# Kernel tuning notes

Measured on AMD Instinct MI355X. Metric: run time of the kernel, lower is better.

## Reference

```python
import jax, jax.numpy as jnp
import numpy as np

B, T, C = 4, 2048, 2048
N_HEAD, N_KV = 16, 4
HEAD_DIM = C // N_HEAD          # 128
KV_DIM = HEAD_DIM * N_KV        # 512
WINDOW = 256
ROPE_BASE = 10000.0


def setup_inputs() -> dict:
    key = jax.random.key(0)
    ks = jax.random.split(key, 5)
    s = 0.02
    return {
        "x": jax.random.normal(ks[0], (B, T, C), dtype=jnp.float32),
        "Wq": jax.random.normal(ks[1], (C, C), dtype=jnp.float32) * s,
        "Wk": jax.random.normal(ks[2], (C, KV_DIM), dtype=jnp.float32) * s,
        "Wv": jax.random.normal(ks[3], (C, KV_DIM), dtype=jnp.float32) * s,
        "Wo": jax.random.normal(ks[4], (C, C), dtype=jnp.float32) * s,
    }


def _rope(x):
    # x: [B, H, T, D]; GPT-NeoX half-split rotation
    d = x.shape[-1]
    t = x.shape[-2]
    inv_freq = 1.0 / (ROPE_BASE ** (jnp.arange(0, d, 2, dtype=jnp.float32) / d))
    freqs = jnp.arange(t, dtype=jnp.float32)[:, None] * inv_freq[None, :]  # [T, D/2]
    cos, sin = jnp.cos(freqs), jnp.sin(freqs)
    x1, x2 = x[..., : d // 2], x[..., d // 2:]
    return jnp.concatenate([x1 * cos - x2 * sin, x1 * sin + x2 * cos], axis=-1)


def reference(x, Wq, Wk, Wv, Wo):
    b, t, c = x.shape
    hd = HEAD_DIM
    q = (x @ Wq).reshape(b, t, N_HEAD, hd).transpose(0, 2, 1, 3)   # [B,nh,T,hd]
    k = (x @ Wk).reshape(b, t, N_KV, hd).transpose(0, 2, 1, 3)     # [B,nkv,T,hd]
    v = (x @ Wv).reshape(b, t, N_KV, hd).transpose(0, 2, 1, 3)

    q = _rope(q)
    k = _rope(k)

    # GQA: repeat kv heads to match query heads
    rep = N_HEAD // N_KV
    k = jnp.repeat(k, rep, axis=1)   # [B,nh,T,hd]
    v = jnp.repeat(v, rep, axis=1)

    att = jnp.einsum("bhqd,bhkd->bhqk", q, k) / jnp.sqrt(jnp.float32(hd))
    i = jnp.arange(t)[:, None]
    j = jnp.arange(t)[None, :]
    # causal AND sliding window: i - WINDOW <= j <= i
    mask = (j <= i) & (j >= i - WINDOW)
    att = jnp.where(mask[None, None], att, jnp.finfo(att.dtype).min)
    att = jax.nn.softmax(att, axis=-1)

    y = jnp.einsum("bhqk,bhkd->bhqd", att, v)          # [B,nh,T,hd]
    y = y.transpose(0, 2, 1, 3).reshape(b, t, c)       # [B,T,C]
    return y @ Wo
```

## Files before the change

### kernel.cpp

```cpp
#include <hip/hip_runtime.h>
#include <stdint.h>

#define T_ 2048
#define C_ 2048
#define HD 128
#define LDQKV 3072

typedef unsigned short u16;
typedef __attribute__((ext_vector_type(8))) short bf16x8;
typedef __attribute__((ext_vector_type(4))) float f32x4;
typedef __attribute__((ext_vector_type(4))) float float4v;
typedef __attribute__((ext_vector_type(4))) u16 u16x4;
typedef __attribute__((ext_vector_type(8))) u16 u16x8;

typedef __attribute__((address_space(3))) void lds_void;
typedef const __attribute__((address_space(1))) void gbl_void;

__device__ __forceinline__ void gload_lds16(const void* g, void* l) {
  __builtin_amdgcn_global_load_lds((gbl_void*)(uintptr_t)g,
                                   (lds_void*)(uint32_t)(uintptr_t)l, 16, 0, 0);
}

__device__ __forceinline__ u16 f2bf(float f) {
  union { float f; uint32_t u; } v; v.f = f;
  uint32_t r = v.u + 0x7FFFu + ((v.u >> 16) & 1u);
  return (u16)(r >> 16);
}
__device__ __forceinline__ float bf2f(u16 h) {
  union { uint32_t u; float f; } v; v.u = ((uint32_t)h) << 16;
  return v.f;
}

#define BAR() do { asm volatile("" ::: "memory"); __builtin_amdgcn_s_barrier(); asm volatile("" ::: "memory"); } while (0)
#define VMCNT(n) asm volatile("s_waitcnt vmcnt(" #n ")" ::: "memory")
template<int N> __device__ __forceinline__ void VMCNT_C() {
  if constexpr (N == 0) { VMCNT(0); }
  else if constexpr (N == 3) { VMCNT(3); }
  else if constexpr (N == 4) { VMCNT(4); }
  else { static_assert(N == 0 || N == 3 || N == 4, "add literal"); }
}

__global__ __launch_bounds__(256) void k_conv_x(const float* __restrict__ x, u16* __restrict__ o) {
  size_t idx = (size_t)blockIdx.x * 256 + threadIdx.x;
  float4v xv = *(const float4v*)(x + idx * 4);
  u16x4 r;
#pragma unroll
  for (int e = 0; e < 4; ++e) r[e] = f2bf(xv[e]);
  *(u16x4*)(o + idx * 4) = r;
}

__device__ __forceinline__ void ttile(const float* __restrict__ src, int ldw, int nb,
                                      int k0, int n0out, u16* __restrict__ out, int tid,
                                      float (*Lt)[68]) {
  int kr = tid >> 4, nc = (tid & 15) * 4;
#pragma unroll
  for (int s = 0; s < 4; ++s) {
    float4v v = *(const float4v*)(src + (size_t)(k0 + kr + 16 * s) * ldw + nb + nc);
#pragma unroll
    for (int e = 0; e < 4; ++e) Lt[kr + 16 * s][nc + e] = v[e];
  }
  __syncthreads();
  int nr = tid & 31, kc = (tid >> 5) * 8;
#pragma unroll
  for (int s2 = 0; s2 < 2; ++s2) {
    int n = nr + 32 * s2;
    u16x8 o;
#pragma unroll
    for (int e = 0; e < 8; ++e) o[e] = f2bf(Lt[kc + e][n]);
    *(u16x8*)(out + (size_t)(n0out + n) * 2048 + k0 + kc) = o;
  }
}

__global__ __launch_bounds__(256) void k_wt_qkv(const float* __restrict__ Wq, const float* __restrict__ Wk,
                                                const float* __restrict__ Wv, u16* __restrict__ wt) {
  __shared__ float Lt[64][68];
  const int n0 = blockIdx.x * 64, k0 = blockIdx.y * 64;
  const float* src; int ldw, nb;
  if (n0 < 2048)      { src = Wq; ldw = 2048; nb = n0; }
  else if (n0 < 2560) { src = Wk; ldw = 512;  nb = n0 - 2048; }
  else                { src = Wv; ldw = 512;  nb = n0 - 2560; }
  ttile(src, ldw, nb, k0, n0, wt, threadIdx.x, Lt);
}

__global__ __launch_bounds__(256) void k_wo_t(const float* __restrict__ Wo, u16* __restrict__ wt) {
  __shared__ float Lt[64][68];
  ttile(Wo, 2048, blockIdx.x * 64, blockIdx.y * 64, blockIdx.x * 64, wt, threadIdx.x, Lt);
}

__global__ __launch_bounds__(256) void k_cs(float* __restrict__ cst) {
  int idx = blockIdx.x * 256 + threadIdx.x;
  int t = idx >> 6, d = idx & 63;
  float inv = expf(-(float)d * (1.0f / 64.0f) * 9.2103403719761836f);
  float f = (float)t * inv;
  float s, c;
  sincosf(f, &s, &c);
  cst[idx * 2] = c;
  cst[idx * 2 + 1] = s;
}

__global__ __launch_bounds__(256) void k_rope(u16* __restrict__ qkv, const float* __restrict__ cst) {
  int idx = blockIdx.x * 256 + threadIdx.x;
  int token = idx / 160;
  int rem = idx - token * 160;
  int hd = rem >> 3, oct = rem & 7;
  int col = ((hd < 16) ? hd * 128 : 2048 + (hd - 16) * 128) + oct * 8;
  size_t base = (size_t)token * LDQKV + col;
  int t = token & (T_ - 1);
  float sc = (hd < 16) ? 0.08838834764831845f : 1.0f;
  u16x8 a = *(const u16x8*)(qkv + base);
  u16x8 b2 = *(const u16x8*)(qkv + base + 64);
  const float* cp = cst + (size_t)(t * 64 + oct * 8) * 2;
  u16x8 ra, rb;
#pragma unroll
  for (int e = 0; e < 8; ++e) {
    float c = cp[e * 2], s = cp[e * 2 + 1];
    float x1 = bf2f(a[e]), x2 = bf2f(b2[e]);
    ra[e] = f2bf((x1 * c - x2 * s) * sc);
    rb[e] = f2bf((x1 * s + x2 * c) * sc);
  }
  *(u16x8*)(qkv + base) = ra;
  *(u16x8*)(qkv + base + 64) = rb;
}

template<int OUTF32, int NF>
__global__ __launch_bounds__(512, 1) void k_gemm8(const u16* __restrict__ A, const u16* __restrict__ Bt,
                                                  void* __restrict__ Cout, int M, int N, int K, int nbx) {
  constexpr int BUFE = 16384 + NF * 4096;
  __shared__ __attribute__((aligned(16))) u16 lds[2 * BUFE];
  const int tid = threadIdx.x, lane = tid & 63;
  const int w = tid >> 6, wm = w >> 2, wn = w & 3;
  const int l15 = lane & 15, lhi = lane >> 4;
  const int nwg = gridDim.x, cpx = nwg >> 3;
  const int wg = (blockIdx.x & 7) * cpx + (blockIdx.x >> 3);
  const int bx = wg % nbx, by = wg / nbx;
  const int m0 = by * 256, n0 = bx * (NF * 64);
  const int NT = K >> 6;

  const int srow = tid >> 3;
  const int scol = ((tid & 7) ^ (srow & 7)) * 8;
  const u16* pA0 = A + (size_t)(m0 + srow) * K + scol;
  const u16* pA1 = pA0 + (size_t)64 * K;
  const u16* pA2 = pA0 + (size_t)128 * K;
  const u16* pA3 = pA0 + (size_t)192 * K;
  const u16* pB0 = Bt + (size_t)(n0 + srow) * K + scol;
  const u16* pB1 = pB0 + (size_t)64 * K;
  const u16* pB2 = pB0 + (size_t)128 * K;
  const u16* pB3 = pB0 + (size_t)(NF == 4 ? 192 : 128) * K;
  u16* dEA = lds + tid * 8;
  u16* dEB = lds + 16384 + tid * 8;
  u16* dOA = lds + BUFE + tid * 8;
  u16* dOB = lds + BUFE + 16384 + tid * 8;
  const int xk0 = (lhi ^ (l15 & 7)) * 8;
  const int xk1 = ((4 + lhi) ^ (l15 & 7)) * 8;
  const u16* rAe0 = lds + (wm * 128 + l15) * 64 + xk0;
  const u16* rAe1 = lds + (wm * 128 + l15) * 64 + xk1;
  const u16* rBe0 = lds + 16384 + (wn * (NF * 16) + l15) * 64 + xk0;
  const u16* rBe1 = lds + 16384 + (wn * (NF * 16) + l15) * 64 + xk1;
  const u16* rAo0 = rAe0 + BUFE;
  const u16* rAo1 = rAe1 + BUFE;
  const u16* rBo0 = rBe0 + BUFE;
  const u16* rBo1 = rBe1 + BUFE;

  f32x4 acc[8][NF];
#pragma unroll
  for (int i = 0; i < 8; ++i)
#pragma unroll
    for (int j = 0; j < NF; ++j) acc[i][j] = (f32x4){0.f, 0.f, 0.f, 0.f};

  gload_lds16(pA0, dEA);         gload_lds16(pA1, dEA + 4096);
  gload_lds16(pA2, dEA + 8192);  gload_lds16(pA3, dEA + 12288);
  gload_lds16(pB0, dEB);         gload_lds16(pB1, dEB + 4096);
  gload_lds16(pB2, dEB + 8192);
  if constexpr (NF == 4) gload_lds16(pB3, dEB + 12288);
  pB0 += 64; pB1 += 64; pB2 += 64;
  if constexpr (NF == 4) pB3 += 64;
  gload_lds16(pB0, dOB);         gload_lds16(pB1, dOB + 4096);
  gload_lds16(pB2, dOB + 8192);
  if constexpr (NF == 4) gload_lds16(pB3, dOB + 12288);
  VMCNT_C<NF>();
  BAR();

  auto TILE = [&](const u16* rA0, const u16* rA1, const u16* rB0, const u16* rB1,
                  u16* dA, u16* dB, bool stA, bool nlast) {
    bf16x8 bb[NF][2], aa[4][2];
    auto MH = [&](int h) {
#pragma unroll
      for (int ks = 0; ks < 2; ++ks)
#pragma unroll
        for (int mi = 0; mi < 4; ++mi)
#pragma unroll
          for (int nf = 0; nf < NF; ++nf)
            acc[h * 4 + mi][nf] = __builtin_amdgcn_mfma_f32_16x16x32_bf16(
                aa[mi][ks], bb[nf][ks], acc[h * 4 + mi][nf], 0, 0, 0);
    };
#pragma unroll
    for (int nf = 0; nf < NF; ++nf) {
      bb[nf][0] = *(const bf16x8*)(rB0 + nf * 1024);
      bb[nf][1] = *(const bf16x8*)(rB1 + nf * 1024);
    }
#pragma unroll
    for (int mi = 0; mi < 4; ++mi) {
      aa[mi][0] = *(const bf16x8*)(rA0 + mi * 1024);
      aa[mi][1] = *(const bf16x8*)(rA1 + mi * 1024);
    }
    if (stA) {
      pA0 += 64; pA1 += 64; pA2 += 64; pA3 += 64;
      gload_lds16(pA0, dA);        gload_lds16(pA1, dA + 4096);
      gload_lds16(pA2, dA + 8192); gload_lds16(pA3, dA + 12288);
    }
    __builtin_amdgcn_s_setprio(1);
    MH(0);
    __builtin_amdgcn_s_setprio(0);
    BAR();
#pragma unroll
    for (int mi = 0; mi < 4; ++mi) {
      aa[mi][0] = *(const bf16x8*)(rA0 + 4096 + mi * 1024);
      aa[mi][1] = *(const bf16x8*)(rA1 + 4096 + mi * 1024);
    }
    if (nlast) {
      pB0 += 64; pB1 += 64; pB2 += 64;
      gload_lds16(pB0, dB);        gload_lds16(pB1, dB + 4096);
      gload_lds16(pB2, dB + 8192);
      if constexpr (NF == 4) { pB3 += 64; gload_lds16(pB3, dB + 12288); }
    }
    __builtin_amdgcn_s_setprio(1);
    MH(1);
    __builtin_amdgcn_s_setprio(0);
    if (nlast) { VMCNT_C<NF>(); } else { VMCNT_C<0>(); }
    BAR();
  };

  for (int t = 0; t < NT; t += 2) {
    const bool nlast = (t + 2 < NT);
    TILE(rAe0, rAe1, rBe0, rBe1, dOA, dEB, true,  nlast);
    TILE(rAo0, rAo1, rBo0, rBo1, dEA, dOB, nlast, nlast);
  }

#pragma unroll
  for (int mf = 0; mf < 8; ++mf) {
#pragma unroll
    for (int nf = 0; nf < NF; ++nf) {
      int col = n0 + wn * (NF * 16) + nf * 16 + l15;
#pragma unroll
      for (int r = 0; r < 4; ++r) {
        int row = m0 + wm * 128 + mf * 16 + lhi * 4 + r;
        float v = acc[mf][nf][r];
        if (OUTF32) ((float*)Cout)[(size_t)row * N + col] = v;
        else        ((u16*)Cout)[(size_t)row * N + col] = f2bf(v);
      }
    }
  }
}

__global__ __launch_bounds__(256) void k_attn(const u16* __restrict__ qkv, u16* __restrict__ y) {
  const int bid = blockIdx.x;
  const int qt = bid & 31, h = (bid >> 5) & 15, b = bid >> 9;
  const int i0 = qt * 64;
  const size_t tb = (size_t)b * T_ * LDQKV;
  const u16* qb = qkv + tb + h * HD;
  const u16* kb = qkv + tb + 2048 + (h >> 2) * HD;
  const u16* vb = kb + 512;
  __shared__ __attribute__((aligned(16))) u16 smem[20480];
  u16* Ks = smem;
  u16* Vt = smem + 8192;
  u16* Psw = smem + 16384;
  u16* Qs = smem;
  const int tid = threadIdx.x, lane = tid & 63, w = tid >> 6;
  const int l15 = lane & 15, lhi = lane >> 4;
  u16* Ps = Psw + w * 1024;

#pragma unroll
  for (int it = 0; it < 4; ++it) {
    int c = it * 256 + tid, row = c >> 4, kc = (c & 15) ^ (row & 7);
    gload_lds16(qb + (size_t)(i0 + row) * LDQKV + kc * 8, &Qs[(it * 256 + w * 64) * 8]);
  }
  __syncthreads();
  bf16x8 qf[4];
#pragma unroll
  for (int ks = 0; ks < 4; ++ks) {
    int row = w * 16 + l15;
    int kc = (ks * 4 + lhi) ^ (row & 7);
    qf[ks] = *(const bf16x8*)&Qs[(row * 16 + kc) * 8];
  }
  __syncthreads();

  f32x4 o[8];
#pragma unroll
  for (int dt = 0; dt < 8; ++dt) o[dt] = (f32x4){0.f, 0.f, 0.f, 0.f};
  float mrun[4], lrun[4];
#pragma unroll
  for (int r = 0; r < 4; ++r) { mrun[r] = -1e30f; lrun[r] = 0.f; }

  const int jb0 = (i0 >= 256) ? (i0 - 256) : 0;
  for (int jb = jb0; jb <= i0; jb += 64) {
#pragma unroll
    for (int it = 0; it < 4; ++it) {
      int c = it * 256 + tid, row = c >> 4, kc = (c & 15) ^ (row & 7);
      gload_lds16(kb + (size_t)(jb + row) * LDQKV + kc * 8, &Ks[(it * 256 + w * 64) * 8]);
    }
#pragma unroll
    for (int it = 0; it < 4; ++it) {
      int chunk = it * 256 + tid, row = chunk >> 4, dc = chunk & 15;
      u16x8 vv = *(const u16x8*)(vb + (size_t)(jb + row) * LDQKV + dc * 8);
#pragma unroll
      for (int e = 0; e < 8; ++e) {
        int d = dc * 8 + e;
        int s = (dc ^ e) & 7;
        Vt[d * 64 + (row ^ (s << 3))] = vv[e];
      }
    }
    __syncthreads();

    f32x4 s[4];
#pragma unroll
    for (int t = 0; t < 4; ++t) {
      s[t] = (f32x4){0.f, 0.f, 0.f, 0.f};
#pragma unroll
      for (int ks = 0; ks < 4; ++ks) {
        int row = t * 16 + l15;
        int kc = (ks * 4 + lhi) ^ (row & 7);
        bf16x8 kf = *(const bf16x8*)&Ks[(row * 16 + kc) * 8];
        s[t] = __builtin_amdgcn_mfma_f32_16x16x32_bf16(qf[ks], kf, s[t], 0, 0, 0);
      }
    }

    const int irow0 = i0 + w * 16 + lhi * 4;
    float rmax[4];
#pragma unroll
    for (int r = 0; r < 4; ++r) rmax[r] = -1e30f;
#pragma unroll
    for (int t = 0; t < 4; ++t) {
      int j = jb + t * 16 + l15;
#pragma unroll
      for (int r = 0; r < 4; ++r) {
        int i = irow0 + r;
        float sv = s[t][r];
        sv = (j <= i && j + 256 >= i) ? sv : -1e30f;
        s[t][r] = sv;
        rmax[r] = fmaxf(rmax[r], sv);
      }
    }
#pragma unroll
    for (int r = 0; r < 4; ++r) {
#pragma unroll
      for (int off = 1; off < 16; off <<= 1)
        rmax[r] = fmaxf(rmax[r], __shfl_xor(rmax[r], off));
    }
    float sf[4], psum[4];
#pragma unroll
    for (int r = 0; r < 4; ++r) {
      float mn = fmaxf(mrun[r], rmax[r]);
      sf[r] = __expf(mrun[r] - mn);
      mrun[r] = mn;
      psum[r] = 0.f;
    }
#pragma unroll
    for (int t = 0; t < 4; ++t) {
#pragma unroll
      for (int r = 0; r < 4; ++r) {
        float p = __expf(s[t][r] - mrun[r]);
        psum[r] += p;
        int q = lhi * 4 + r;
        int k = t * 16 + l15;
        Ps[q * 64 + (k ^ ((q & 7) << 3))] = f2bf(p);
      }
    }
#pragma unroll
    for (int r = 0; r < 4; ++r) {
#pragma unroll
      for (int off = 1; off < 16; off <<= 1)
        psum[r] += __shfl_xor(psum[r], off);
      lrun[r] = lrun[r] * sf[r] + psum[r];
    }
#pragma unroll
    for (int dt = 0; dt < 8; ++dt)
#pragma unroll
      for (int r = 0; r < 4; ++r)
        o[dt][r] = o[dt][r] * sf[r];

    bf16x8 pf[2];
#pragma unroll
    for (int ks2 = 0; ks2 < 2; ++ks2)
      pf[ks2] = *(const bf16x8*)&Ps[l15 * 64 + ((ks2 * 32 + lhi * 8) ^ ((l15 & 7) << 3))];
#pragma unroll
    for (int dt = 0; dt < 8; ++dt) {
#pragma unroll
      for (int ks2 = 0; ks2 < 2; ++ks2) {
        int d = dt * 16 + l15;
        int s2 = ((d >> 3) ^ (d & 7)) & 7;
        bf16x8 vf = *(const bf16x8*)&Vt[d * 64 + ((ks2 * 32 + lhi * 8) ^ (s2 << 3))];
        o[dt] = __builtin_amdgcn_mfma_f32_16x16x32_bf16(pf[ks2], vf, o[dt], 0, 0, 0);
      }
    }
    __syncthreads();
  }

#pragma unroll
  for (int dt = 0; dt < 8; ++dt) {
#pragma unroll
    for (int r = 0; r < 4; ++r) {
      int i = i0 + w * 16 + lhi * 4 + r;
      float v = o[dt][r] / lrun[r];
      y[((size_t)b * T_ + i) * C_ + h * HD + dt * 16 + l15] = f2bf(v);
    }
  }
}

extern "C" void kernel_launch(void* const* d_in, const int* in_sizes, int n_in,
                              void* d_out, int out_size, void* d_ws, size_t ws_size,
                              hipStream_t stream) {
  const float* x  = (const float*)d_in[0];
  const float* Wq = (const float*)d_in[1];
  const float* Wk = (const float*)d_in[2];
  const float* Wv = (const float*)d_in[3];
  const float* Wo = (const float*)d_in[4];
  char* ws = (char*)d_ws;
  u16* x_bf   = (u16*)(ws);
  u16* wt_qkv = (u16*)(ws + 33554432);
  u16* wo_t   = (u16*)(ws + 46137344);
  u16* qkv    = (u16*)(ws + 54525952);
  float* cst  = (float*)(ws + 104857600);
  u16* ybuf = x_bf;

  k_conv_x <<<16384, 256, 0, stream>>>(x, x_bf);
  k_wt_qkv <<<dim3(48, 32), 256, 0, stream>>>(Wq, Wk, Wv, wt_qkv);
  k_wo_t   <<<dim3(32, 32), 256, 0, stream>>>(Wo, wo_t);
  k_cs     <<<512, 256, 0, stream>>>(cst);

  k_gemm8<0, 3><<<512, 512, 0, stream>>>(x_bf, wt_qkv, (void*)qkv, 8192, 3072, 2048, 16);

  k_rope   <<<5120, 256, 0, stream>>>(qkv, cst);
  k_attn   <<<2048, 256, 0, stream>>>(qkv, ybuf);

  k_gemm8<1, 4><<<256, 512, 0, stream>>>(ybuf, wo_t, d_out, 8192, 2048, 2048, 8);
}
```

Baseline: 295.3 us.

## Merge prep kernels into one launch and fuse RoPE into QKV GEMM epilogue

Four preprocessing kernels (x conversion, two weight transposes, cos/sin table) become one kernel that dispatches on block index. The separate RoPE pass is folded into the QKV GEMM epilogue. The B-row loads are permuted so each rotation pair lands in adjacent columns, and the partner value is fetched with a lane shuffle. This removes three launches and a full read/write pass over the q/k buffer. The cost is extra epilogue work and cos/sin table loads, plus an interleaved q/k column order that attention must tolerate, so correctness depends on that layout.

```diff
diff --git a/kernel.cpp b/kernel.cpp
--- a/kernel.cpp
+++ b/kernel.cpp
@@ -40,15 +40,6 @@
   else { static_assert(N == 0 || N == 3 || N == 4, "add literal"); }
 }
 
-__global__ __launch_bounds__(256) void k_conv_x(const float* __restrict__ x, u16* __restrict__ o) {
-  size_t idx = (size_t)blockIdx.x * 256 + threadIdx.x;
-  float4v xv = *(const float4v*)(x + idx * 4);
-  u16x4 r;
-#pragma unroll
-  for (int e = 0; e < 4; ++e) r[e] = f2bf(xv[e]);
-  *(u16x4*)(o + idx * 4) = r;
-}
-
 __device__ __forceinline__ void ttile(const float* __restrict__ src, int ldw, int nb,
                                       int k0, int n0out, u16* __restrict__ out, int tid,
                                       float (*Lt)[68]) {
@@ -71,60 +62,47 @@
   }
 }
 
-__global__ __launch_bounds__(256) void k_wt_qkv(const float* __restrict__ Wq, const float* __restrict__ Wk,
-                                                const float* __restrict__ Wv, u16* __restrict__ wt) {
+__global__ __launch_bounds__(256) void k_prep(const float* __restrict__ x,
+                                              const float* __restrict__ Wq, const float* __restrict__ Wk,
+                                              const float* __restrict__ Wv, const float* __restrict__ Wo,
+                                              u16* __restrict__ xbf, u16* __restrict__ wtq,
+                                              u16* __restrict__ wot, float* __restrict__ cst) {
   __shared__ float Lt[64][68];
-  const int n0 = blockIdx.x * 64, k0 = blockIdx.y * 64;
-  const float* src; int ldw, nb;
-  if (n0 < 2048)      { src = Wq; ldw = 2048; nb = n0; }
-  else if (n0 < 2560) { src = Wk; ldw = 512;  nb = n0 - 2048; }
-  else                { src = Wv; ldw = 512;  nb = n0 - 2560; }
-  ttile(src, ldw, nb, k0, n0, wt, threadIdx.x, Lt);
-}
-
-__global__ __launch_bounds__(256) void k_wo_t(const float* __restrict__ Wo, u16* __restrict__ wt) {
-  __shared__ float Lt[64][68];
-  ttile(Wo, 2048, blockIdx.x * 64, blockIdx.y * 64, blockIdx.x * 64, wt, threadIdx.x, Lt);
-}
-
-__global__ __launch_bounds__(256) void k_cs(float* __restrict__ cst) {
-  int idx = blockIdx.x * 256 + threadIdx.x;
-  int t = idx >> 6, d = idx & 63;
-  float inv = expf(-(float)d * (1.0f / 64.0f) * 9.2103403719761836f);
-  float f = (float)t * inv;
-  float s, c;
-  sincosf(f, &s, &c);
-  cst[idx * 2] = c;
-  cst[idx * 2 + 1] = s;
-}
-
-__global__ __launch_bounds__(256) void k_rope(u16* __restrict__ qkv, const float* __restrict__ cst) {
-  int idx = blockIdx.x * 256 + threadIdx.x;
-  int token = idx / 160;
-  int rem = idx - token * 160;
-  int hd = rem >> 3, oct = rem & 7;
-  int col = ((hd < 16) ? hd * 128 : 2048 + (hd - 16) * 128) + oct * 8;
-  size_t base = (size_t)token * LDQKV + col;
-  int t = token & (T_ - 1);
-  float sc = (hd < 16) ? 0.08838834764831845f : 1.0f;
-  u16x8 a = *(const u16x8*)(qkv + base);
-  u16x8 b2 = *(const u16x8*)(qkv + base + 64);
-  const float* cp = cst + (size_t)(t * 64 + oct * 8) * 2;
-  u16x8 ra, rb;
-#pragma unroll
-  for (int e = 0; e < 8; ++e) {
-    float c = cp[e * 2], s = cp[e * 2 + 1];
-    float x1 = bf2f(a[e]), x2 = bf2f(b2[e]);
-    ra[e] = f2bf((x1 * c - x2 * s) * sc);
-    rb[e] = f2bf((x1 * s + x2 * c) * sc);
-  }
-  *(u16x8*)(qkv + base) = ra;
-  *(u16x8*)(qkv + base + 64) = rb;
-}
-
-template<int OUTF32, int NF>
+  const int bid = blockIdx.x, tid = threadIdx.x;
+  if (bid < 16384) {
+    size_t idx = (size_t)bid * 256 + tid;
+    float4v xv = *(const float4v*)(x + idx * 4);
+    u16x4 r;
+#pragma unroll
+    for (int e = 0; e < 4; ++e) r[e] = f2bf(xv[e]);
+    *(u16x4*)(xbf + idx * 4) = r;
+  } else if (bid < 17920) {
+    int b = bid - 16384;
+    int n0 = (b % 48) * 64, k0 = (b / 48) * 64;
+    const float* src; int ldw, nb;
+    if (n0 < 2048)      { src = Wq; ldw = 2048; nb = n0; }
+    else if (n0 < 2560) { src = Wk; ldw = 512;  nb = n0 - 2048; }
+    else                { src = Wv; ldw = 512;  nb = n0 - 2560; }
+    ttile(src, ldw, nb, k0, n0, wtq, tid, Lt);
+  } else if (bid < 18944) {
+    int b = bid - 17920;
+    ttile(Wo, 2048, (b % 32) * 64, (b / 32) * 64, (b % 32) * 64, wot, tid, Lt);
+  } else {
+    int idx = (bid - 18944) * 256 + tid;
+    int t = idx >> 6, d = idx & 63;
+    float inv = expf(-(float)d * (1.0f / 64.0f) * 9.2103403719761836f);
+    float f = (float)t * inv;
+    float s, c;
+    sincosf(f, &s, &c);
+    cst[idx * 2] = c;
+    cst[idx * 2 + 1] = s;
+  }
+}
+
+template<int OUTF32, int NF, int ROPE>
 __global__ __launch_bounds__(512, 1) void k_gemm8(const u16* __restrict__ A, const u16* __restrict__ Bt,
-                                                  void* __restrict__ Cout, int M, int N, int K, int nbx) {
+                                                  void* __restrict__ Cout, const float* __restrict__ cst,
+                                                  int M, int N, int K, int nbx) {
   constexpr int BUFE = 16384 + NF * 4096;
   __shared__ __attribute__((aligned(16))) u16 lds[2 * BUFE];
   const int tid = threadIdx.x, lane = tid & 63;
@@ -136,16 +114,23 @@
   const int m0 = by * 256, n0 = bx * (NF * 64);
   const int NT = K >> 6;
 
+  auto prow = [&](int n) -> int {
+    if constexpr (ROPE) {
+      if (n < 2560) { int hc = n & 127; return (n & ~127) | ((hc >> 1) + ((hc & 1) << 6)); }
+    }
+    return n;
+  };
+
   const int srow = tid >> 3;
   const int scol = ((tid & 7) ^ (srow & 7)) * 8;
   const u16* pA0 = A + (size_t)(m0 + srow) * K + scol;
   const u16* pA1 = pA0 + (size_t)64 * K;
   const u16* pA2 = pA0 + (size_t)128 * K;
   const u16* pA3 = pA0 + (size_t)192 * K;
-  const u16* pB0 = Bt + (size_t)(n0 + srow) * K + scol;
-  const u16* pB1 = pB0 + (size_t)64 * K;
-  const u16* pB2 = pB0 + (size_t)128 * K;
-  const u16* pB3 = pB0 + (size_t)(NF == 4 ? 192 : 128) * K;
+  const u16* pB0 = Bt + (size_t)prow(n0 + srow) * K + scol;
+  const u16* pB1 = Bt + (size_t)prow(n0 + 64 + srow) * K + scol;
+  const u16* pB2 = Bt + (size_t)prow(n0 + 128 + srow) * K + scol;
+  const u16* pB3 = Bt + (size_t)prow(n0 + (NF == 4 ? 192 : 128) + srow) * K + scol;
   u16* dEA = lds + tid * 8;
   u16* dEB = lds + 16384 + tid * 8;
   u16* dOA = lds + BUFE + tid * 8;
@@ -241,10 +226,27 @@
 #pragma unroll
     for (int nf = 0; nf < NF; ++nf) {
       int col = n0 + wn * (NF * 16) + nf * 16 + l15;
+      bool qk = false;
+      float sc = 1.0f, sgn = 1.0f;
+      int dcol = 0;
+      if constexpr (ROPE) {
+        qk = (col < 2560);
+        sc = (col < 2048) ? 0.08838834764831845f : 1.0f;
+        sgn = (col & 1) ? 1.0f : -1.0f;
+        dcol = (col & 127) >> 1;
+      }
 #pragma unroll
       for (int r = 0; r < 4; ++r) {
         int row = m0 + wm * 128 + mf * 16 + lhi * 4 + r;
-        float v = acc[mf][nf][r];
+        float a = acc[mf][nf][r];
+        float v = a;
+        if constexpr (ROPE) {
+          if (qk) {
+            float b = __shfl_xor(a, 1);
+            const float* cp = cst + (size_t)(((row & 2047) << 6) + dcol) * 2;
+            v = (a * cp[0] + b * sgn * cp[1]) * sc;
+          }
+        }
         if (OUTF32) ((float*)Cout)[(size_t)row * N + col] = v;
         else        ((u16*)Cout)[(size_t)row * N + col] = f2bf(v);
       }
@@ -422,15 +424,11 @@
   float* cst  = (float*)(ws + 104857600);
   u16* ybuf = x_bf;
 
-  k_conv_x <<<16384, 256, 0, stream>>>(x, x_bf);
-  k_wt_qkv <<<dim3(48, 32), 256, 0, stream>>>(Wq, Wk, Wv, wt_qkv);
-  k_wo_t   <<<dim3(32, 32), 256, 0, stream>>>(Wo, wo_t);
-  k_cs     <<<512, 256, 0, stream>>>(cst);
-
-  k_gemm8<0, 3><<<512, 512, 0, stream>>>(x_bf, wt_qkv, (void*)qkv, 8192, 3072, 2048, 16);
-
-  k_rope   <<<5120, 256, 0, stream>>>(qkv, cst);
-  k_attn   <<<2048, 256, 0, stream>>>(qkv, ybuf);
-
-  k_gemm8<1, 4><<<256, 512, 0, stream>>>(ybuf, wo_t, d_out, 8192, 2048, 2048, 8);
-}
+  k_prep<<<19456, 256, 0, stream>>>(x, Wq, Wk, Wv, Wo, x_bf, wt_qkv, wo_t, cst);
+
+  k_gemm8<0, 3, 1><<<512, 512, 0, stream>>>(x_bf, wt_qkv, (void*)qkv, cst, 8192, 3072, 2048, 16);
+
+  k_attn<<<2048, 256, 0, stream>>>(qkv, ybuf);
+
+  k_gemm8<1, 4, 0><<<256, 512, 0, stream>>>(ybuf, wo_t, d_out, nullptr, 8192, 2048, 2048, 8);
+}
```

Measured after the change: 302.8 us. 1.03x slower.
